# Performance work log

Measured on AMD Instinct MI355X. Metric: run time of the kernel, lower is better.

## Reference

```python
import jax, jax.numpy as jnp
import numpy as np
from jax import lax

N_ANGLES = 1000
N_DET = 513
S_RANGE = 0.13
IMG = 512
CROP = 362


def setup_inputs() -> dict:
    key = jax.random.key(0)
    x = jax.random.normal(key, (8, 1, N_ANGLES, N_DET), dtype=jnp.float32)
    return {"x": x}


def reference(x):
    # x: (B, 1, A, D) filtered sinogram
    B = x.shape[0]
    delta_s = 2.0 * S_RANGE / (N_DET - 1)
    lin = jnp.linspace(-S_RANGE, S_RANGE, IMG)
    # torch: Y, X = meshgrid(x, y, indexing='ij') -> Y varies along rows, X along cols
    Y = lin[:, None]   # (IMG, 1)
    X = lin[None, :]   # (1, IMG)
    theta = jnp.linspace(0.0, jnp.pi, N_ANGLES + 1)[:-1]
    cos_t = jnp.cos(theta)
    sin_t = jnp.sin(theta)

    sino = jnp.swapaxes(x[:, 0], 0, 1)  # (A, B, D)

    def body(acc, inp):
        c, s, row = inp  # row: (B, D)
        # detector position (pixels, align_corners=True) for every image pixel
        p = (X * c + Y * s + S_RANGE) / delta_s          # (IMG, IMG)
        i0 = jnp.floor(p).astype(jnp.int32)
        w = (p - i0).astype(x.dtype)
        i1 = i0 + 1
        # grid_sample padding_mode='zeros': OOB taps contribute 0
        v0 = jnp.where((i0 >= 0) & (i0 < N_DET),
                       row[:, jnp.clip(i0, 0, N_DET - 1)], 0.0)  # (B, IMG, IMG)
        v1 = jnp.where((i1 >= 0) & (i1 < N_DET),
                       row[:, jnp.clip(i1, 0, N_DET - 1)], 0.0)
        acc = acc + v0 * (1.0 - w) + v1 * w
        return acc, None

    acc0 = jnp.zeros((B, IMG, IMG), dtype=x.dtype)
    acc, _ = lax.scan(body, acc0, (cos_t, sin_t, sino))

    top = (IMG - CROP) // 2
    out = acc[:, top:top + CROP, top:top + CROP] * (jnp.pi / N_ANGLES)
    out = jnp.swapaxes(out, -1, -2)  # final transpose as in torch forward
    return out[:, None]  # (B, 1, CROP, CROP)
```

## Files before the change

### kernel.cpp

```cpp
#include <hip/hip_runtime.h>

#define NA 1000
#define NCH 4
#define CHMAX 256
#define ND 513
#define ND2 512
#define CROP 362
#define TOP 75
#define NPIX (CROP * CROP)
#define NTILE 23
#define GRP 8
#define WIN 32

typedef __fp16 half2_t __attribute__((ext_vector_type(2)));

__device__ float2 g_tab[NA];
__device__ uint4  g_plo[(size_t)NA * ND2];
__device__ uint4  g_phi[(size_t)NA * ND2];
__device__ float  g_part[(size_t)NCH * 8 * NPIX];

__global__ void table_kernel() {
    int a = blockIdx.x * blockDim.x + threadIdx.x;
    if (a >= NA) return;
    double th = (double)a * (3.14159265358979323846 / (double)NA);
    float delta_f = (float)(2.0 * 0.13 / (double)(ND - 1));
    double inv = 1.0 / (double)delta_f;
    g_tab[a] = make_float2((float)(cos(th) * inv), (float)(sin(th) * inv));
}

__global__ void pack_kernel(const float* __restrict__ x) {
    int t = blockIdx.x * blockDim.x + threadIdx.x;
    if (t >= NA * ND2) return;
    int a = t >> 9, d = t & 511;
    const float* p0 = x + (size_t)a * ND + d;
    const int S = NA * ND;
    unsigned int lo[4], hi[4];
    #pragma unroll
    for (int b = 0; b < 4; ++b) {
        half2_t h;
        h.x = (__fp16)p0[(size_t)b * S];
        h.y = (__fp16)p0[(size_t)b * S + 1];
        __builtin_memcpy(&lo[b], &h, 4);
        half2_t g;
        g.x = (__fp16)p0[(size_t)(b + 4) * S];
        g.y = (__fp16)p0[(size_t)(b + 4) * S + 1];
        __builtin_memcpy(&hi[b], &g, 4);
    }
    g_plo[t] = make_uint4(lo[0], lo[1], lo[2], lo[3]);
    g_phi[t] = make_uint4(hi[0], hi[1], hi[2], hi[3]);
}

__device__ __forceinline__ float dot2(unsigned int pair, half2_t wp, float acc) {
    half2_t h; __builtin_memcpy(&h, &pair, 4);
    float d;
    asm("v_dot2_f32_f16 %0, %1, %2, %3" : "=v"(d) : "v"(h), "v"(wp), "v"(acc));
    return d;
}

__global__ __launch_bounds__(256, 8) void bp_kernel() {
    __shared__ uint4 s_lo[2][GRP * WIN];
    __shared__ uint4 s_hi[2][GRP * WIN];
    __shared__ int   s_base[CHMAX];

    int ch  = blockIdx.z;
    int A0  = ch << 8;
    int len = min(CHMAX, NA - A0);
    int ngrp = len >> 3;
    int tid = threadIdx.x;
    int bi  = blockIdx.y, bj = blockIdx.x;

    const float step = (float)(0.26 / 511.0);

    float Xa = fmaf((float)(TOP + bi * 16),      step, -0.13f);
    float Xb = fmaf((float)(TOP + bi * 16 + 15), step, -0.13f);
    float Ya = fmaf((float)(TOP + bj * 16),      step, -0.13f);
    float Yb = fmaf((float)(TOP + bj * 16 + 15), step, -0.13f);
    for (int aidx = tid; aidx < len; aidx += 256) {
        float2 cs = g_tab[A0 + aidx];
        float p0 = fmaf(Xa, cs.x, fmaf(Ya, cs.y, 256.0f));
        float p1 = fmaf(Xb, cs.x, fmaf(Ya, cs.y, 256.0f));
        float p2 = fmaf(Xa, cs.x, fmaf(Yb, cs.y, 256.0f));
        float p3 = fmaf(Xb, cs.x, fmaf(Yb, cs.y, 256.0f));
        float pm = fminf(fminf(p0, p1), fminf(p2, p3)) - 2.0f;
        int b = (int)floorf(pm);
        b = b < 0 ? 0 : b;
        b = b > (ND2 - WIN) ? (ND2 - WIN) : b;
        s_base[aidx] = b;
    }
    __syncthreads();

    int wave = tid >> 6, lane = tid & 63;
    int i = bi * 16 + (wave >> 1) * 8 + (lane >> 3);
    int j = bj * 16 + (wave & 1) * 8 + (lane & 7);
    int ic = min(i, CROP - 1), jc = min(j, CROP - 1);
    float X = fmaf((float)(TOP + ic), step, -0.13f);
    float Y = fmaf((float)(TOP + jc), step, -0.13f);

    double dth = 3.14159265358979323846 / 1000.0;
    float delta_f = (float)(2.0 * 0.13 / (double)(ND - 1));
    double invd = 1.0 / (double)delta_f;
    float c0 = (float)(cos((A0 + 0) * dth) * invd), s0r = (float)(sin((A0 + 0) * dth) * invd);
    float c1 = (float)(cos((A0 + 1) * dth) * invd), s1r = (float)(sin((A0 + 1) * dth) * invd);
    float c2 = (float)(cos((A0 + 2) * dth) * invd), s2r = (float)(sin((A0 + 2) * dth) * invd);
    float c3 = (float)(cos((A0 + 3) * dth) * invd), s3r = (float)(sin((A0 + 3) * dth) * invd);
    float C4 = (float)cos(4.0 * dth), S4 = (float)sin(4.0 * dth);

    int sk = tid >> 5, sl = tid & 31;

    {
        size_t idx = (size_t)(A0 + sk) * ND2 + s_base[sk] + sl;
        s_lo[0][tid] = g_plo[idx];
        s_hi[0][tid] = g_phi[idx];
    }
    __syncthreads();

    float acc0 = 0.f, acc1 = 0.f, acc2 = 0.f, acc3 = 0.f;
    float acc4 = 0.f, acc5 = 0.f, acc6 = 0.f, acc7 = 0.f;

#define BODY(K, BASE, CC, SS)                                           \
    {                                                                   \
        float p  = fmaf(X, CC, fmaf(Y, SS, 256.0f));                    \
        float fi = floorf(p);                                           \
        half2_t wp = __builtin_amdgcn_cvt_pkrtz(fi - p + 1.0f, p - fi); \
        int l = (int)fi - (BASE);                                       \
        uint4 lo = blo[(K) * WIN + l];                                  \
        uint4 hi = bhi[(K) * WIN + l];                                  \
        acc0 = dot2(lo.x, wp, acc0);                                    \
        acc1 = dot2(lo.y, wp, acc1);                                    \
        acc2 = dot2(lo.z, wp, acc2);                                    \
        acc3 = dot2(lo.w, wp, acc3);                                    \
        acc4 = dot2(hi.x, wp, acc4);                                    \
        acc5 = dot2(hi.y, wp, acc5);                                    \
        acc6 = dot2(hi.z, wp, acc6);                                    \
        acc7 = dot2(hi.w, wp, acc7);                                    \
        float oc = CC, os = SS;                                         \
        float m1 = os * S4; CC = fmaf(oc, C4, -m1);                     \
        float m2 = os * C4; SS = fmaf(oc, S4, m2);                      \
    }

    for (int g = 0; g < ngrp; ++g) {
        int cur = g & 1;
        bool have = (g + 1) < ngrp;
        uint4 r0, r1;
        if (have) {
            int ag = (g + 1) * GRP + sk;
            size_t idx = (size_t)(A0 + ag) * ND2 + s_base[ag] + sl;
            r0 = g_plo[idx];
            r1 = g_phi[idx];
        }

        const uint4* blo = s_lo[cur];
        const uint4* bhi = s_hi[cur];
        int gb = g * GRP;
        #pragma unroll
        for (int q = 0; q < 2; ++q) {
            int4 b4 = *(const int4*)(s_base + gb + q * 4);
            BODY(q * 4 + 0, b4.x, c0, s0r)
            BODY(q * 4 + 1, b4.y, c1, s1r)
            BODY(q * 4 + 2, b4.z, c2, s2r)
            BODY(q * 4 + 3, b4.w, c3, s3r)
        }

        if (have) {
            int nxt = cur ^ 1;
            s_lo[nxt][tid] = r0;
            s_hi[nxt][tid] = r1;
        }
        __syncthreads();
    }
#undef BODY

    if (i < CROP && j < CROP) {
        float* p0 = g_part + (size_t)ch * 8 * NPIX + (size_t)i * CROP + j;
        p0[0 * NPIX] = acc0; p0[1 * NPIX] = acc1;
        p0[2 * NPIX] = acc2; p0[3 * NPIX] = acc3;
        p0[4 * NPIX] = acc4; p0[5 * NPIX] = acc5;
        p0[6 * NPIX] = acc6; p0[7 * NPIX] = acc7;
    }
}

__global__ void combine_kernel(float* __restrict__ out) {
    int t = blockIdx.x * 256 + threadIdx.x;
    if (t >= 8 * NPIX) return;
    const float scale = (float)(3.14159265358979323846 / 1000.0);
    float s = 0.f;
    #pragma unroll
    for (int ch = 0; ch < NCH; ++ch) s += g_part[(size_t)ch * 8 * NPIX + t];
    out[t] = s * scale;
}

extern "C" void kernel_launch(void* const* d_in, const int* in_sizes, int n_in,
                              void* d_out, int out_size, void* d_ws, size_t ws_size,
                              hipStream_t stream) {
    const float* x = (const float*)d_in[0];
    float* out = (float*)d_out;

    table_kernel<<<(NA + 255) / 256, 256, 0, stream>>>();
    pack_kernel<<<(NA * ND2 + 255) / 256, 256, 0, stream>>>(x);

    dim3 bgrid(NTILE, NTILE, NCH);
    bp_kernel<<<bgrid, 256, 0, stream>>>();

    combine_kernel<<<(8 * NPIX + 255) / 256, 256, 0, stream>>>(out);
}
```

Baseline: 124.0 us.

## Serve batches 6-7 from global gathers, read angle table from LDS, use 3 chunks

The packed sinogram is split three ways: batches 0-3 and 4-5 are staged in LDS, while batches 6-7 go to a separate array that each pixel gathers straight from global memory through the caches. Per-angle cos/sin are read from a shared copy of the table, and angles 4-7 of each group come from rotating angles 0-3, replacing the running rotation. The angle range is cut into 3 chunks of 336 instead of 4 of 256, giving fewer partial sums and blocks. The goal is to cut LDS staging traffic and per-group work. The cost is per-pixel scattered global loads that depend on cache hit rates, and fewer blocks to spread across the GPU.

After: 165.2 us (median of 4 runs). +33.2%, slower.

```diff
diff --git a/kernel.cpp b/kernel.cpp
--- a/kernel.cpp
+++ b/kernel.cpp
@@ -1,8 +1,8 @@
 #include <hip/hip_runtime.h>
 
 #define NA 1000
-#define NCH 4
-#define CHMAX 256
+#define NCH 3
+#define CHMAX 336
 #define ND 513
 #define ND2 512
 #define CROP 362
@@ -12,11 +12,15 @@
 #define GRP 8
 #define WIN 32
 
+#define C4R 0.9999210442038161f
+#define S4R 0.0125660398933523f
+
 typedef __fp16 half2_t __attribute__((ext_vector_type(2)));
 
 __device__ float2 g_tab[NA];
 __device__ uint4  g_plo[(size_t)NA * ND2];
-__device__ uint4  g_phi[(size_t)NA * ND2];
+__device__ uint2  g_pmid[(size_t)NA * ND2];
+__device__ uint2  g_p67[(size_t)NA * ND2];
 __device__ float  g_part[(size_t)NCH * 8 * NPIX];
 
 __global__ void table_kernel() {
@@ -34,20 +38,17 @@
     int a = t >> 9, d = t & 511;
     const float* p0 = x + (size_t)a * ND + d;
     const int S = NA * ND;
-    unsigned int lo[4], hi[4];
+    unsigned int w[8];
     #pragma unroll
-    for (int b = 0; b < 4; ++b) {
+    for (int b = 0; b < 8; ++b) {
         half2_t h;
         h.x = (__fp16)p0[(size_t)b * S];
         h.y = (__fp16)p0[(size_t)b * S + 1];
-        __builtin_memcpy(&lo[b], &h, 4);
-        half2_t g;
-        g.x = (__fp16)p0[(size_t)(b + 4) * S];
-        g.y = (__fp16)p0[(size_t)(b + 4) * S + 1];
-        __builtin_memcpy(&hi[b], &g, 4);
-    }
-    g_plo[t] = make_uint4(lo[0], lo[1], lo[2], lo[3]);
-    g_phi[t] = make_uint4(hi[0], hi[1], hi[2], hi[3]);
+        __builtin_memcpy(&w[b], &h, 4);
+    }
+    g_plo[t]  = make_uint4(w[0], w[1], w[2], w[3]);
+    g_pmid[t] = make_uint2(w[4], w[5]);
+    g_p67[t]  = make_uint2(w[6], w[7]);
 }
 
 __device__ __forceinline__ float dot2(unsigned int pair, half2_t wp, float acc) {
@@ -58,12 +59,13 @@
 }
 
 __global__ __launch_bounds__(256, 8) void bp_kernel() {
-    __shared__ uint4 s_lo[2][GRP * WIN];
-    __shared__ uint4 s_hi[2][GRP * WIN];
-    __shared__ int   s_base[CHMAX];
+    __shared__ uint4  s_lo[2][GRP * WIN];
+    __shared__ uint2  s_mid[2][GRP * WIN];
+    __shared__ float2 s_tab[CHMAX];
+    __shared__ int    s_base[CHMAX];
 
     int ch  = blockIdx.z;
-    int A0  = ch << 8;
+    int A0  = ch * CHMAX;
     int len = min(CHMAX, NA - A0);
     int ngrp = len >> 3;
     int tid = threadIdx.x;
@@ -77,6 +79,7 @@
     float Yb = fmaf((float)(TOP + bj * 16 + 15), step, -0.13f);
     for (int aidx = tid; aidx < len; aidx += 256) {
         float2 cs = g_tab[A0 + aidx];
+        s_tab[aidx] = cs;
         float p0 = fmaf(Xa, cs.x, fmaf(Ya, cs.y, 256.0f));
         float p1 = fmaf(Xb, cs.x, fmaf(Ya, cs.y, 256.0f));
         float p2 = fmaf(Xa, cs.x, fmaf(Yb, cs.y, 256.0f));
@@ -96,21 +99,12 @@
     float X = fmaf((float)(TOP + ic), step, -0.13f);
     float Y = fmaf((float)(TOP + jc), step, -0.13f);
 
-    double dth = 3.14159265358979323846 / 1000.0;
-    float delta_f = (float)(2.0 * 0.13 / (double)(ND - 1));
-    double invd = 1.0 / (double)delta_f;
-    float c0 = (float)(cos((A0 + 0) * dth) * invd), s0r = (float)(sin((A0 + 0) * dth) * invd);
-    float c1 = (float)(cos((A0 + 1) * dth) * invd), s1r = (float)(sin((A0 + 1) * dth) * invd);
-    float c2 = (float)(cos((A0 + 2) * dth) * invd), s2r = (float)(sin((A0 + 2) * dth) * invd);
-    float c3 = (float)(cos((A0 + 3) * dth) * invd), s3r = (float)(sin((A0 + 3) * dth) * invd);
-    float C4 = (float)cos(4.0 * dth), S4 = (float)sin(4.0 * dth);
-
     int sk = tid >> 5, sl = tid & 31;
 
     {
         size_t idx = (size_t)(A0 + sk) * ND2 + s_base[sk] + sl;
-        s_lo[0][tid] = g_plo[idx];
-        s_hi[0][tid] = g_phi[idx];
+        s_lo[0][tid]  = g_plo[idx];
+        s_mid[0][tid] = g_pmid[idx];
     }
     __syncthreads();
 
@@ -121,50 +115,63 @@
     {                                                                   \
         float p  = fmaf(X, CC, fmaf(Y, SS, 256.0f));                    \
         float fi = floorf(p);                                           \
-        half2_t wp = __builtin_amdgcn_cvt_pkrtz(fi - p + 1.0f, p - fi); \
-        int l = (int)fi - (BASE);                                       \
+        float w  = p - fi;                                              \
+        half2_t wp = __builtin_amdgcn_cvt_pkrtz(1.0f - w, w);           \
+        int i0 = (int)fi;                                               \
+        int l  = i0 - (BASE);                                           \
         uint4 lo = blo[(K) * WIN + l];                                  \
-        uint4 hi = bhi[(K) * WIN + l];                                  \
+        uint2 md = bmd[(K) * WIN + l];                                  \
+        uint2 hi = grow[((K) << 9) + i0];                               \
         acc0 = dot2(lo.x, wp, acc0);                                    \
         acc1 = dot2(lo.y, wp, acc1);                                    \
         acc2 = dot2(lo.z, wp, acc2);                                    \
         acc3 = dot2(lo.w, wp, acc3);                                    \
-        acc4 = dot2(hi.x, wp, acc4);                                    \
-        acc5 = dot2(hi.y, wp, acc5);                                    \
-        acc6 = dot2(hi.z, wp, acc6);                                    \
-        acc7 = dot2(hi.w, wp, acc7);                                    \
-        float oc = CC, os = SS;                                         \
-        float m1 = os * S4; CC = fmaf(oc, C4, -m1);                     \
-        float m2 = os * C4; SS = fmaf(oc, S4, m2);                      \
+        acc4 = dot2(md.x, wp, acc4);                                    \
+        acc5 = dot2(md.y, wp, acc5);                                    \
+        acc6 = dot2(hi.x, wp, acc6);                                    \
+        acc7 = dot2(hi.y, wp, acc7);                                    \
     }
 
     for (int g = 0; g < ngrp; ++g) {
         int cur = g & 1;
         bool have = (g + 1) < ngrp;
-        uint4 r0, r1;
+        uint4 r0; uint2 r1;
         if (have) {
             int ag = (g + 1) * GRP + sk;
             size_t idx = (size_t)(A0 + ag) * ND2 + s_base[ag] + sl;
             r0 = g_plo[idx];
-            r1 = g_phi[idx];
+            r1 = g_pmid[idx];
         }
 
         const uint4* blo = s_lo[cur];
-        const uint4* bhi = s_hi[cur];
+        const uint2* bmd = s_mid[cur];
         int gb = g * GRP;
-        #pragma unroll
-        for (int q = 0; q < 2; ++q) {
-            int4 b4 = *(const int4*)(s_base + gb + q * 4);
-            BODY(q * 4 + 0, b4.x, c0, s0r)
-            BODY(q * 4 + 1, b4.y, c1, s1r)
-            BODY(q * 4 + 2, b4.z, c2, s2r)
-            BODY(q * 4 + 3, b4.w, c3, s3r)
-        }
+        const uint2* __restrict__ grow = g_p67 + ((size_t)(A0 + gb) << 9);
+
+        int4  b4a = *(const int4*)(s_base + gb);
+        int4  b4b = *(const int4*)(s_base + gb + 4);
+        float4 t01 = *(const float4*)(s_tab + gb);
+        float4 t23 = *(const float4*)(s_tab + gb + 2);
+        float c_0 = t01.x, s_0 = t01.y, c_1 = t01.z, s_1 = t01.w;
+        float c_2 = t23.x, s_2 = t23.y, c_3 = t23.z, s_3 = t23.w;
+        float c_4 = fmaf(c_0, C4R, -(s_0 * S4R)), s_4 = fmaf(c_0, S4R, s_0 * C4R);
+        float c_5 = fmaf(c_1, C4R, -(s_1 * S4R)), s_5 = fmaf(c_1, S4R, s_1 * C4R);
+        float c_6 = fmaf(c_2, C4R, -(s_2 * S4R)), s_6 = fmaf(c_2, S4R, s_2 * C4R);
+        float c_7 = fmaf(c_3, C4R, -(s_3 * S4R)), s_7 = fmaf(c_3, S4R, s_3 * C4R);
+
+        BODY(0, b4a.x, c_0, s_0)
+        BODY(1, b4a.y, c_1, s_1)
+        BODY(2, b4a.z, c_2, s_2)
+        BODY(3, b4a.w, c_3, s_3)
+        BODY(4, b4b.x, c_4, s_4)
+        BODY(5, b4b.y, c_5, s_5)
+        BODY(6, b4b.z, c_6, s_6)
+        BODY(7, b4b.w, c_7, s_7)
 
         if (have) {
             int nxt = cur ^ 1;
-            s_lo[nxt][tid] = r0;
-            s_hi[nxt][tid] = r1;
+            s_lo[nxt][tid]  = r0;
+            s_mid[nxt][tid] = r1;
         }
         __syncthreads();
     }
```

## Use direct global-to-LDS loads and rebalance angle chunks to three

Applied to the files above, without the earlier changes.

Prefetches of the next angle group now go straight from global memory into shared memory through the global_load_lds builtin, removing the register staging and the separate LDS store. The angle split drops from 4 chunks of 256 to 3 chunks of 336, which cuts the partial-sum writes and the combine reads but reduces the grid from 2116 to 1587 blocks. Initial angle coefficients come from the precomputed table instead of per-thread double-precision trig. The risks are lower parallelism per launch and a memory-ordering hazard, since the LDS writes from global_load_lds may not be waited on before the barrier.

Result: slower. 127.4 us (+2.7%).

```diff
diff --git a/kernel.cpp b/kernel.cpp
--- a/kernel.cpp
+++ b/kernel.cpp
@@ -1,8 +1,8 @@
 #include <hip/hip_runtime.h>
 
 #define NA 1000
-#define NCH 4
-#define CHMAX 256
+#define NCH 3
+#define CH0 336
 #define ND 513
 #define ND2 512
 #define CROP 362
@@ -12,7 +12,22 @@
 #define GRP 8
 #define WIN 32
 
+#define C4R 0.9999210442038161f
+#define S4R 0.0125660398933523f
+
 typedef __fp16 half2_t __attribute__((ext_vector_type(2)));
+
+#if defined(__has_builtin)
+#if __has_builtin(__builtin_amdgcn_global_load_lds)
+#define HAS_GLL 1
+#endif
+#endif
+
+#ifdef HAS_GLL
+#define GLL(G, L) __builtin_amdgcn_global_load_lds(                        \
+    (const __attribute__((address_space(1))) void*)(G),                   \
+    (__attribute__((address_space(3))) void*)(L), 16, 0, 0)
+#endif
 
 __device__ float2 g_tab[NA];
 __device__ uint4  g_plo[(size_t)NA * ND2];
@@ -57,14 +72,16 @@
     return d;
 }
 
+#define ROT4(CC, SS) { float oc=CC, os=SS; CC = fmaf(oc, C4R, -(os*S4R)); SS = fmaf(oc, S4R, os*C4R); }
+
 __global__ __launch_bounds__(256, 8) void bp_kernel() {
     __shared__ uint4 s_lo[2][GRP * WIN];
     __shared__ uint4 s_hi[2][GRP * WIN];
-    __shared__ int   s_base[CHMAX];
+    __shared__ alignas(16) int s_base[CH0];
 
     int ch  = blockIdx.z;
-    int A0  = ch << 8;
-    int len = min(CHMAX, NA - A0);
+    int A0  = ch * CH0;
+    int len = min(CH0, NA - A0);
     int ngrp = len >> 3;
     int tid = threadIdx.x;
     int bi  = blockIdx.y, bj = blockIdx.x;
@@ -75,8 +92,8 @@
     float Xb = fmaf((float)(TOP + bi * 16 + 15), step, -0.13f);
     float Ya = fmaf((float)(TOP + bj * 16),      step, -0.13f);
     float Yb = fmaf((float)(TOP + bj * 16 + 15), step, -0.13f);
-    for (int aidx = tid; aidx < len; aidx += 256) {
-        float2 cs = g_tab[A0 + aidx];
+    for (int t = tid; t < len; t += 256) {
+        float2 cs = g_tab[A0 + t];
         float p0 = fmaf(Xa, cs.x, fmaf(Ya, cs.y, 256.0f));
         float p1 = fmaf(Xb, cs.x, fmaf(Ya, cs.y, 256.0f));
         float p2 = fmaf(Xa, cs.x, fmaf(Yb, cs.y, 256.0f));
@@ -85,7 +102,7 @@
         int b = (int)floorf(pm);
         b = b < 0 ? 0 : b;
         b = b > (ND2 - WIN) ? (ND2 - WIN) : b;
-        s_base[aidx] = b;
+        s_base[t] = b;
     }
     __syncthreads();
 
@@ -96,79 +113,92 @@
     float X = fmaf((float)(TOP + ic), step, -0.13f);
     float Y = fmaf((float)(TOP + jc), step, -0.13f);
 
-    double dth = 3.14159265358979323846 / 1000.0;
-    float delta_f = (float)(2.0 * 0.13 / (double)(ND - 1));
-    double invd = 1.0 / (double)delta_f;
-    float c0 = (float)(cos((A0 + 0) * dth) * invd), s0r = (float)(sin((A0 + 0) * dth) * invd);
-    float c1 = (float)(cos((A0 + 1) * dth) * invd), s1r = (float)(sin((A0 + 1) * dth) * invd);
-    float c2 = (float)(cos((A0 + 2) * dth) * invd), s2r = (float)(sin((A0 + 2) * dth) * invd);
-    float c3 = (float)(cos((A0 + 3) * dth) * invd), s3r = (float)(sin((A0 + 3) * dth) * invd);
-    float C4 = (float)cos(4.0 * dth), S4 = (float)sin(4.0 * dth);
-
-    int sk = tid >> 5, sl = tid & 31;
+    int sk = tid >> 5, sc = tid & 31;
+    int wb = tid & 192;
+
+    float2 t0 = g_tab[A0 + 0], t1 = g_tab[A0 + 1];
+    float2 t2 = g_tab[A0 + 2], t3 = g_tab[A0 + 3];
+    float c_0 = t0.x, s_0 = t0.y, c_1 = t1.x, s_1 = t1.y;
+    float c_2 = t2.x, s_2 = t2.y, c_3 = t3.x, s_3 = t3.y;
 
     {
-        size_t idx = (size_t)(A0 + sk) * ND2 + s_base[sk] + sl;
+        size_t idx = (size_t)(A0 + sk) * ND2 + s_base[sk] + sc;
+#ifdef HAS_GLL
+        GLL(g_plo + idx, &s_lo[0][wb]);
+        GLL(g_phi + idx, &s_hi[0][wb]);
+#else
         s_lo[0][tid] = g_plo[idx];
         s_hi[0][tid] = g_phi[idx];
+#endif
     }
     __syncthreads();
 
     float acc0 = 0.f, acc1 = 0.f, acc2 = 0.f, acc3 = 0.f;
     float acc4 = 0.f, acc5 = 0.f, acc6 = 0.f, acc7 = 0.f;
 
-#define BODY(K, BASE, CC, SS)                                           \
+#define LBODY(K, BASE, CC, SS)                                          \
     {                                                                   \
         float p  = fmaf(X, CC, fmaf(Y, SS, 256.0f));                    \
         float fi = floorf(p);                                           \
-        half2_t wp = __builtin_amdgcn_cvt_pkrtz(fi - p + 1.0f, p - fi); \
-        int l = (int)fi - (BASE);                                       \
-        uint4 lo = blo[(K) * WIN + l];                                  \
-        uint4 hi = bhi[(K) * WIN + l];                                  \
-        acc0 = dot2(lo.x, wp, acc0);                                    \
-        acc1 = dot2(lo.y, wp, acc1);                                    \
-        acc2 = dot2(lo.z, wp, acc2);                                    \
-        acc3 = dot2(lo.w, wp, acc3);                                    \
-        acc4 = dot2(hi.x, wp, acc4);                                    \
-        acc5 = dot2(hi.y, wp, acc5);                                    \
-        acc6 = dot2(hi.z, wp, acc6);                                    \
-        acc7 = dot2(hi.w, wp, acc7);                                    \
-        float oc = CC, os = SS;                                         \
-        float m1 = os * S4; CC = fmaf(oc, C4, -m1);                     \
-        float m2 = os * C4; SS = fmaf(oc, S4, m2);                      \
+        float w  = p - fi;                                              \
+        half2_t wp = __builtin_amdgcn_cvt_pkrtz(1.0f - w, w);           \
+        int l = (int)fi - (BASE) + (K) * WIN;                           \
+        uint4 A = blo[l];                                               \
+        uint4 B = bhi[l];                                               \
+        acc0 = dot2(A.x, wp, acc0);                                     \
+        acc1 = dot2(A.y, wp, acc1);                                     \
+        acc2 = dot2(A.z, wp, acc2);                                     \
+        acc3 = dot2(A.w, wp, acc3);                                     \
+        acc4 = dot2(B.x, wp, acc4);                                     \
+        acc5 = dot2(B.y, wp, acc5);                                     \
+        acc6 = dot2(B.z, wp, acc6);                                     \
+        acc7 = dot2(B.w, wp, acc7);                                     \
     }
 
     for (int g = 0; g < ngrp; ++g) {
         int cur = g & 1;
         bool have = (g + 1) < ngrp;
+#ifndef HAS_GLL
         uint4 r0, r1;
+#endif
         if (have) {
-            int ag = (g + 1) * GRP + sk;
-            size_t idx = (size_t)(A0 + ag) * ND2 + s_base[ag] + sl;
+            int ag = ((g + 1) << 3) + sk;
+            size_t idx = (size_t)(A0 + ag) * ND2 + s_base[ag] + sc;
+#ifdef HAS_GLL
+            GLL(g_plo + idx, &s_lo[cur ^ 1][wb]);
+            GLL(g_phi + idx, &s_hi[cur ^ 1][wb]);
+#else
             r0 = g_plo[idx];
             r1 = g_phi[idx];
+#endif
         }
 
         const uint4* blo = s_lo[cur];
         const uint4* bhi = s_hi[cur];
-        int gb = g * GRP;
-        #pragma unroll
-        for (int q = 0; q < 2; ++q) {
-            int4 b4 = *(const int4*)(s_base + gb + q * 4);
-            BODY(q * 4 + 0, b4.x, c0, s0r)
-            BODY(q * 4 + 1, b4.y, c1, s1r)
-            BODY(q * 4 + 2, b4.z, c2, s2r)
-            BODY(q * 4 + 3, b4.w, c3, s3r)
+        int gb = g << 3;
+        int4 b4a = *(const int4*)(s_base + gb);
+        int4 b4b = *(const int4*)(s_base + gb + 4);
+
+        LBODY(0, b4a.x, c_0, s_0)
+        LBODY(1, b4a.y, c_1, s_1)
+        LBODY(2, b4a.z, c_2, s_2)
+        LBODY(3, b4a.w, c_3, s_3)
+        ROT4(c_0, s_0) ROT4(c_1, s_1) ROT4(c_2, s_2) ROT4(c_3, s_3)
+        LBODY(4, b4b.x, c_0, s_0)
+        LBODY(5, b4b.y, c_1, s_1)
+        LBODY(6, b4b.z, c_2, s_2)
+        LBODY(7, b4b.w, c_3, s_3)
+        ROT4(c_0, s_0) ROT4(c_1, s_1) ROT4(c_2, s_2) ROT4(c_3, s_3)
+
+#ifndef HAS_GLL
+        if (have) {
+            s_lo[cur ^ 1][tid] = r0;
+            s_hi[cur ^ 1][tid] = r1;
         }
-
-        if (have) {
-            int nxt = cur ^ 1;
-            s_lo[nxt][tid] = r0;
-            s_hi[nxt][tid] = r1;
-        }
+#endif
         __syncthreads();
     }
-#undef BODY
+#undef LBODY
 
     if (i < CROP && j < CROP) {
         float* p0 = g_part + (size_t)ch * 8 * NPIX + (size_t)i * CROP + j;
```
